# Performance work log

Hardware: AMD Instinct MI355X
Metric: run time of the kernel (lower is better)

Reference implementation:

```python
import jax, jax.numpy as jnp
import numpy as np

HIDDEN = 2560
NUM_HEADS = 32
HEAD = HIDDEN // NUM_HEADS  # 80
ROT = 32                    # partial rotary dim (phi)
THETA = 10000.0
B, S = 2, 2048


def _apply_rope(x, pos):
    """Neox-style rotary embedding on the first ROT dims of the head.
    x: [B, S, H, HEAD], pos: [B, S] int."""
    inv_freq = 1.0 / (THETA ** (jnp.arange(0, ROT, 2, dtype=jnp.float32) / ROT))  # [ROT/2]
    freqs = pos.astype(jnp.float32)[..., None] * inv_freq  # [B, S, ROT/2]
    cos = jnp.cos(freqs)[:, :, None, :].astype(x.dtype)    # [B, S, 1, ROT/2]
    sin = jnp.sin(freqs)[:, :, None, :].astype(x.dtype)
    x_rot, x_pass = x[..., :ROT], x[..., ROT:]
    x1, x2 = x_rot[..., :ROT // 2], x_rot[..., ROT // 2:]
    rotated = jnp.concatenate([x1 * cos - x2 * sin, x2 * cos + x1 * sin], axis=-1)
    return jnp.concatenate([rotated, x_pass], axis=-1)


def setup_inputs() -> dict:
    key = jax.random.key(0)
    k0, k1, k2 = jax.random.split(key, 3)
    hidden_states = jax.random.normal(k0, (B, S, HIDDEN), dtype=jnp.float32)
    position_ids = jnp.broadcast_to(jnp.arange(S, dtype=jnp.int32), (B, S))
    Wqkv_w = jax.random.normal(k1, (3 * HIDDEN, HIDDEN), dtype=jnp.float32) * 0.02
    Wqkv_b = jnp.zeros((3 * HIDDEN,), dtype=jnp.float32)
    out_w = jax.random.normal(k2, (HIDDEN, HIDDEN), dtype=jnp.float32) * 0.02
    out_b = jnp.zeros((HIDDEN,), dtype=jnp.float32)
    return {"position_ids": position_ids, "hidden_states": hidden_states,
            "Wqkv_w": Wqkv_w, "Wqkv_b": Wqkv_b, "out_w": out_w, "out_b": out_b}


def reference(position_ids, hidden_states, Wqkv_w, Wqkv_b, out_w, out_b):
    # Fused QKV projection (torch Linear: y = x @ W^T + b)
    qkv = jnp.einsum('bsh,oh->bso', hidden_states, Wqkv_w) + Wqkv_b  # [B,S,3*HIDDEN]
    q, k, v = jnp.split(qkv, 3, axis=-1)
    q = q.reshape(B, S, NUM_HEADS, HEAD)
    k = k.reshape(B, S, NUM_HEADS, HEAD)
    v = v.reshape(B, S, NUM_HEADS, HEAD)
    # Inline RoPE on q/k (partial, first ROT dims)
    q = _apply_rope(q, position_ids)
    k = _apply_rope(k, position_ids)
    # Causal scaled-dot-product attention (math of the paged prefill kernel)
    scale = HEAD ** -0.5
    scores = jnp.einsum('bqhd,bkhd->bhqk', q, k) * scale  # [B,H,S,S]
    causal = jnp.tril(jnp.ones((S, S), dtype=bool))
    scores = jnp.where(causal, scores, jnp.finfo(scores.dtype).min)
    attn = jax.nn.softmax(scores, axis=-1)
    ctx = jnp.einsum('bhqk,bkhd->bqhd', attn, v).reshape(B, S, HIDDEN)
    return jnp.einsum('bsh,oh->bso', ctx, out_w) + out_b
```

## Files before the change

### kernel.cpp

```cpp
#include <hip/hip_runtime.h>
#include <stdint.h>

#define HIDDEN  2560
#define NHEADS  32
#define HEAD    80
#define QKS     96
#define SEQ     2048
#define BATCH   2
#define M_TOTAL (BATCH*SEQ)
#define QKV_N   (3*HIDDEN)
#define PART_SLOTS 36

typedef __attribute__((ext_vector_type(8))) short  short8;
typedef __attribute__((ext_vector_type(4))) float  floatx4;
typedef __attribute__((ext_vector_type(4))) float  fvec4;
typedef __attribute__((ext_vector_type(4))) unsigned short usvec4;
typedef __attribute__((ext_vector_type(2))) unsigned int uint2v;

#define SBAR() __builtin_amdgcn_sched_barrier(0)

__device__ __forceinline__ unsigned short f2bf(float x){
  union { float f; unsigned u; } v; v.f = x;
  unsigned r = v.u + 0x7fffu + ((v.u >> 16) & 1u);
  return (unsigned short)(r >> 16);
}
__device__ __forceinline__ float bf2f(unsigned short h){
  union { unsigned u; float f; } v; v.u = ((unsigned)h) << 16;
  return v.f;
}
__device__ __forceinline__ unsigned cvt_pk_bf16(float lo, float hi){
  unsigned r;
  asm volatile("v_cvt_pk_bf16_f32 %0, %1, %2" : "=v"(r) : "v"(lo), "v"(hi));
  return r;
}
__device__ __forceinline__ void gload16(const void* g, void* l){
  __builtin_amdgcn_global_load_lds(
    (const __attribute__((address_space(1))) void*)g,
    (__attribute__((address_space(3))) void*)l, 16, 0, 0);
}

__global__ __launch_bounds__(256)
void convert_f32_bf16(const float* __restrict__ src, unsigned short* __restrict__ dst, int n4){
  int idx = blockIdx.x*blockDim.x + threadIdx.x;
  int stride = gridDim.x*blockDim.x;
  for (int i = idx; i < n4; i += stride){
    fvec4 v = *(const fvec4*)(src + (size_t)i*4);
    usvec4 o;
    o[0]=f2bf(v[0]); o[1]=f2bf(v[1]); o[2]=f2bf(v[2]); o[3]=f2bf(v[3]);
    *(usvec4*)(dst + (size_t)i*4) = o;
  }
}

template<bool OUT_BF16>
__global__ __launch_bounds__(512, 2)
void gemm256(const unsigned short* __restrict__ A, const unsigned short* __restrict__ Bm,
             const float* __restrict__ bias, void* __restrict__ Cout,
             int M, int N, int K)
{
  __shared__ __align__(16) unsigned short lds[65536];
  const int tid  = threadIdx.x;
  const int lane = tid & 63;
  const int w    = tid >> 6;
  const int wm   = w >> 2;
  const int wn   = w & 3;
  const int l15  = lane & 15, lg = lane >> 4;

  const int gx  = gridDim.x;
  const int lid = blockIdx.y*gx + blockIdx.x;
  const int nwg = gx*gridDim.y;
  const int qch = nwg >> 3;
  const int sl  = (lid & 7)*qch + (lid >> 3);
  const int bn0 = (sl % gx) * 256;
  const int bm0 = (sl / gx) * 256;

  const int nt = K >> 6;

  int rowq[2], cq[2];
  #pragma unroll
  for (int q=0;q<2;q++){
    int u = (w*2+q)*64 + lane;
    rowq[q] = u >> 2;
    cq[q]   = ((u & 3) - (rowq[q] >> 1)) & 3;
  }
  const int rot = (lg + (l15 >> 1)) & 3;

  floatx4 acc[8][4];
  #pragma unroll
  for (int m=0;m<8;m++)
    #pragma unroll
    for (int n=0;n<4;n++) acc[m][n] = (floatx4)0.0f;

  auto STAGE = [&](int tau, int kkh){
    const int bufb = tau & 1;
    const size_t kofs = (size_t)tau*64 + kkh*32;
    const unsigned sA = (unsigned)(((bufb*2 + 0)*2 + kkh) * 8192);
    const unsigned sB = (unsigned)(((bufb*2 + 1)*2 + kkh) * 8192);
    #pragma unroll
    for (int q=0;q<2;q++){
      gload16(A  + (size_t)(bm0 + rowq[q])*K + kofs + cq[q]*8, &lds[sA + (w*2+q)*512]);
      gload16(Bm + (size_t)(bn0 + rowq[q])*K + kofs + cq[q]*8, &lds[sB + (w*2+q)*512]);
    }
  };
  auto COMPUTE = [&](int bufb, int kkh){
    const unsigned short* As = &lds[((bufb*2+0)*2+kkh)*8192];
    const unsigned short* Bs = &lds[((bufb*2+1)*2+kkh)*8192];
    short8 af[8], bfv[4];
    __builtin_amdgcn_s_setprio(1);
    #pragma unroll
    for (int n=0;n<4;n++)
      bfv[n] = *(const short8*)&Bs[(((wn*64 + n*16 + l15)<<2) + rot)*8];
    #pragma unroll
    for (int m=0;m<8;m++)
      af[m] = *(const short8*)&As[(((wm*128 + m*16 + l15)<<2) + rot)*8];
    #pragma unroll
    for (int m=0;m<8;m++)
      #pragma unroll
      for (int n=0;n<4;n++)
        acc[m][n] = __builtin_amdgcn_mfma_f32_16x16x32_bf16(af[m], bfv[n], acc[m][n], 0, 0, 0);
    __builtin_amdgcn_s_setprio(0);
  };

  STAGE(0,0);
  STAGE(0,1);
  STAGE(1,0);
  asm volatile("s_waitcnt vmcnt(8)" ::: "memory");
  __builtin_amdgcn_s_barrier(); SBAR();

  for (int t=0; t<nt; ++t){
    const int c = t & 1;
    if (t+1 < nt) STAGE(t+1, 1);
    COMPUTE(c, 0);
    if (t+1 < nt) asm volatile("s_waitcnt vmcnt(8)" ::: "memory");
    else          asm volatile("s_waitcnt vmcnt(0)" ::: "memory");
    __builtin_amdgcn_s_barrier(); SBAR();
    if (t+2 < nt) STAGE(t+2, 0);
    COMPUTE(c, 1);
    if (t+1 < nt){
      if (t+2 < nt) asm volatile("s_waitcnt vmcnt(8)" ::: "memory");
      else          asm volatile("s_waitcnt vmcnt(4)" ::: "memory");
      __builtin_amdgcn_s_barrier(); SBAR();
    }
  }

  #pragma unroll
  for (int m=0;m<8;m++){
    #pragma unroll
    for (int n=0;n<4;n++){
      int col = bn0 + wn*64 + n*16 + l15;
      float bs = bias[col];
      #pragma unroll
      for (int r=0;r<4;r++){
        int row = bm0 + wm*128 + m*16 + lg*4 + r;
        float v = acc[m][n][r] + bs;
        if (OUT_BF16) ((unsigned short*)Cout)[(size_t)row*N + col] = f2bf(v);
        else          ((float*)Cout)[(size_t)row*N + col] = v;
      }
    }
  }
}

__global__ __launch_bounds__(256)
void rope_scatter(const unsigned short* __restrict__ qkv,
                  const int* __restrict__ pos_ids,
                  unsigned short* __restrict__ Qp, unsigned short* __restrict__ Kp,
                  unsigned short* __restrict__ Vt)
{
  __shared__ float cosb[128*16];
  __shared__ float sinb[128*16];
  __shared__ __align__(16) unsigned short vtile[128*88];
  const int tid = threadIdx.x;
  const int blk = blockIdx.x;
  const int st = blk & 15, h = (blk >> 4) & 31, b = blk >> 9;
  const int s0 = st*128;

  for (int idx = tid; idx < 128*16; idx += 256){
    int sl = idx >> 4, i = idx & 15;
    float p = (float)pos_ids[b*SEQ + s0 + sl];
    float inv = exp2f(-(float)i * (13.287712379549449f/16.0f));
    float ang = p * inv;
    cosb[idx] = cosf(ang);
    sinb[idx] = sinf(ang);
  }
  __syncthreads();

  const size_t qkrow = (size_t)(b*SEQ + s0)*QKV_N;
  const size_t obase = ((size_t)(b*NHEADS + h)*SEQ + s0)*QKS;
  #pragma unroll
  for (int part = 0; part < 2; part++){
    const int cbase = part*HIDDEN + h*HEAD;
    unsigned short* outp = part ? Kp : Qp;
    for (int idx = tid; idx < 128*QKS; idx += 256){
      int sl = idx / QKS, d = idx - sl*QKS;
      const size_t rb = qkrow + (size_t)sl*QKV_N + cbase;
      float v;
      if (d < 16){
        float x1 = bf2f(qkv[rb + d]);
        float x2 = bf2f(qkv[rb + d + 16]);
        v = x1*cosb[sl*16 + d] - x2*sinb[sl*16 + d];
      } else if (d < 32){
        int i = d - 16;
        float x1 = bf2f(qkv[rb + d - 16]);
        float x2 = bf2f(qkv[rb + d]);
        v = x2*cosb[sl*16 + i] + x1*sinb[sl*16 + i];
      } else if (d < HEAD){
        v = bf2f(qkv[rb + d]);
      } else v = 0.0f;
      outp[obase + (size_t)sl*QKS + d] = f2bf(v);
    }
  }

  for (int idx = tid; idx < 128*HEAD; idx += 256){
    int sl = idx / HEAD, d = idx - sl*HEAD;
    vtile[sl*88 + d] = qkv[qkrow + (size_t)sl*QKV_N + 2*HIDDEN + h*HEAD + d];
  }
  __syncthreads();
  const size_t vtb = ((size_t)(b*NHEADS + h)*HEAD)*SEQ + s0;
  for (int idx = tid; idx < HEAD*128; idx += 256){
    int d = idx >> 7, sl = idx & 127;
    Vt[vtb + (size_t)d*SEQ + sl] = vtile[sl*88 + d];
  }
}

__global__ __launch_bounds__(256, 4)
void attn_fd(const unsigned short* __restrict__ Qp,
             const unsigned short* __restrict__ Kp,
             const unsigned short* __restrict__ Vt,
             unsigned short* __restrict__ ctx,
             unsigned short* __restrict__ pO,
             float* __restrict__ pML)
{
  __shared__ __align__(16) unsigned short Klds[2][64*96];
  __shared__ __align__(16) unsigned short Vlds[2][80*64];
  __shared__ __align__(16) unsigned short p_lds[4][32*36];
  const int tid = threadIdx.x;
  const int lane = tid & 63, w = tid >> 6;
  const int l15 = lane & 15, lg = lane >> 4;

  const int bid = blockIdx.x;
  const int xcd = bid & 7, j = bid >> 3;
  const int bh  = (j/40)*8 + xcd;
  const int tr  = j - (j/40)*40;

  int qt, part, np;
  if (tr < 16)      { qt = 12 + (tr>>2); part = tr & 3; np = 4; }
  else if (tr < 28) { int t = tr-16; int q3 = t/3; qt = 8 + q3; part = t - q3*3; np = 3; }
  else if (tr < 36) { int t = tr-28; qt = 4 + (t>>1); part = t & 1; np = 2; }
  else              { qt = tr - 36; part = 0; np = 1; }
  const int nk  = 2*qt + 2;
  const int kt0 = (part*nk)/np, kt1 = ((part+1)*nk)/np;
  const int q0  = qt*128 + w*32;

  const unsigned short* Qb = Qp + ((size_t)bh*SEQ)*QKS;
  const unsigned short* Kb = Kp + ((size_t)bh*SEQ)*QKS;
  const unsigned short* Vb = Vt + ((size_t)bh*HEAD)*SEQ;

  short8 qf[2][3];
  #pragma unroll
  for (int mi=0; mi<2; mi++)
    #pragma unroll
    for (int kc=0; kc<3; kc++)
      qf[mi][kc] = *(const short8*)&Qb[(size_t)(q0 + mi*16 + l15)*QKS + kc*32 + lg*8];

  int ksrow[3], ksc[3];
  #pragma unroll
  for (int t=0;t<3;t++){
    int ci = (w*3 + t)*64 + lane;
    int row = ci/12, c = ci - row*12;
    ksrow[t] = row;
    ksc[t]   = (c ^ (row & 3))*8;
  }
  int vsrow[3], vsc[3];
  #pragma unroll
  for (int t=0;t<3;t++){
    int i = w + 4*t;
    int row = i*8 + (lane >> 3), c = lane & 7;
    vsrow[t] = row;
    vsc[t]   = (c ^ (row & 7))*8;
  }

  auto STAGE_T = [&](int kt, int bb){
    #pragma unroll
    for (int t=0;t<3;t++)
      gload16(Kb + (size_t)(kt*64 + ksrow[t])*QKS + ksc[t], &Klds[bb][(w*3+t)*512]);
    #pragma unroll
    for (int t=0;t<3;t++){
      int i = w + 4*t;
      if (i < 10)
        gload16(Vb + (size_t)vsrow[t]*SEQ + kt*64 + vsc[t], &Vlds[bb][i*512]);
    }
  };

  float mrun[2] = {-3e38f, -3e38f};
  float lrun[2] = {0.0f, 0.0f};
  floatx4 oacc[2][5];
  #pragma unroll
  for (int mi=0;mi<2;mi++)
    #pragma unroll
    for (int di=0;di<5;di++) oacc[mi][di] = (floatx4)0.0f;

  const float SC = 0.1118033988749895f * 1.4426950408889634f;

  STAGE_T(kt0, 0);
  __syncthreads();

  for (int kt = kt0; kt < kt1; kt++){
    const int cur = (kt - kt0) & 1;
    if (kt+1 < kt1) STAGE_T(kt+1, cur^1);

    if (kt*64 <= q0 + 31){
      floatx4 sacc[2][4];
      #pragma unroll
      for (int mi=0;mi<2;mi++)
        #pragma unroll
        for (int ni=0;ni<4;ni++) sacc[mi][ni] = (floatx4)0.0f;

      __builtin_amdgcn_s_setprio(1);
      #pragma unroll
      for (int kc=0; kc<3; kc++){
        short8 kf[4];
        #pragma unroll
        for (int ni=0; ni<4; ni++){
          int r = ni*16 + l15;
          kf[ni] = *(const short8*)&Klds[cur][r*96 + (((kc*4+lg) ^ (r & 3))<<3)];
        }
        #pragma unroll
        for (int mi=0; mi<2; mi++)
          #pragma unroll
          for (int ni=0; ni<4; ni++)
            sacc[mi][ni] = __builtin_amdgcn_mfma_f32_16x16x32_bf16(kf[ni], qf[mi][kc], sacc[mi][ni], 0, 0, 0);
      }
      __builtin_amdgcn_s_setprio(0);

      if (kt*64 + 63 > q0){
        #pragma unroll
        for (int mi=0; mi<2; mi++){
          int qrow = q0 + mi*16 + l15;
          #pragma unroll
          for (int ni=0; ni<4; ni++){
            int kb = kt*64 + ni*16 + lg*4;
            #pragma unroll
            for (int r=0; r<4; r++)
              if (kb + r > qrow) sacc[mi][ni][r] = -3e38f;
          }
        }
      }

      #pragma unroll
      for (int mi=0; mi<2; mi++){
        float pm = -3e38f;
        #pragma unroll
        for (int ni=0; ni<4; ni++)
          #pragma unroll
          for (int r=0; r<4; r++) pm = fmaxf(pm, sacc[mi][ni][r]);
        pm = fmaxf(pm, __shfl_xor(pm, 16));
        pm = fmaxf(pm, __shfl_xor(pm, 32));
        float mold = mrun[mi];
        float mnew = fmaxf(mold, pm);
        float msc  = mnew*SC;
        float alpha = __builtin_amdgcn_exp2f(mold*SC - msc);
        float rs = 0.0f;
        #pragma unroll
        for (int ni=0; ni<4; ni++)
          #pragma unroll
          for (int r=0; r<4; r++){
            float p = __builtin_amdgcn_exp2f(sacc[mi][ni][r]*SC - msc);
            sacc[mi][ni][r] = p;
            rs += p;
          }
        rs += __shfl_xor(rs, 16);
        rs += __shfl_xor(rs, 32);
        lrun[mi] = lrun[mi]*alpha + rs;
        mrun[mi] = mnew;
        #pragma unroll
        for (int di=0; di<5; di++) oacc[mi][di] *= alpha;
      }

      #pragma unroll
      for (int kk=0; kk<2; kk++){
        #pragma unroll
        for (int mi=0; mi<2; mi++)
          #pragma unroll
          for (int nl=0; nl<2; nl++){
            int ni = kk*2 + nl;
            uint2v pk;
            pk[0] = cvt_pk_bf16(sacc[mi][ni][0], sacc[mi][ni][1]);
            pk[1] = cvt_pk_bf16(sacc[mi][ni][2], sacc[mi][ni][3]);
            *(uint2v*)&p_lds[w][(mi*16 + l15)*36 + nl*16 + lg*4] = pk;
          }
        __builtin_amdgcn_s_setprio(1);
        short8 pa[2];
        #pragma unroll
        for (int mi=0;mi<2;mi++)
          pa[mi] = *(const short8*)&p_lds[w][(mi*16 + l15)*36 + lg*8];
        #pragma unroll
        for (int di=0; di<5; di++){
          int r = di*16 + l15;
          short8 vf = *(const short8*)&Vlds[cur][r*64 + (((kk*4+lg) ^ (r & 7))<<3)];
          #pragma unroll
          for (int mi=0;mi<2;mi++)
            oacc[mi][di] = __builtin_amdgcn_mfma_f32_16x16x32_bf16(vf, pa[mi], oacc[mi][di], 0, 0, 0);
        }
        __builtin_amdgcn_s_setprio(0);
      }
    }
    __syncthreads();
  }

  const int b = bh >> 5, h = bh & 31;
  if (np == 1){
    #pragma unroll
    for (int mi=0;mi<2;mi++){
      float inv = 1.0f/lrun[mi];
      size_t crow = ((size_t)(b*SEQ + q0 + mi*16 + l15))*HIDDEN + h*HEAD;
      #pragma unroll
      for (int di=0;di<5;di++){
        uint2v pk;
        pk[0] = cvt_pk_bf16(oacc[mi][di][0]*inv, oacc[mi][di][1]*inv);
        pk[1] = cvt_pk_bf16(oacc[mi][di][2]*inv, oacc[mi][di][3]*inv);
        *(uint2v*)&ctx[crow + di*16 + lg*4] = pk;
      }
    }
  } else {
    int base;
    if (np == 2)      base = (qt-4)*2;
    else if (np == 3) base = 8 + (qt-8)*3;
    else              base = 20 + (qt-12)*4;
    const int pslot = bh*PART_SLOTS + base + part;
    unsigned short* Ob = pO + (size_t)pslot*128*HEAD;
    #pragma unroll
    for (int mi=0;mi<2;mi++){
      int grow = w*32 + mi*16 + l15;
      #pragma unroll
      for (int di=0;di<5;di++){
        uint2v pk;
        pk[0] = cvt_pk_bf16(oacc[mi][di][0], oacc[mi][di][1]);
        pk[1] = cvt_pk_bf16(oacc[mi][di][2], oacc[mi][di][3]);
        *(uint2v*)&Ob[grow*HEAD + di*16 + lg*4] = pk;
      }
      if (lg == 0){
        float* mlb = pML + ((size_t)pslot*128 + grow)*2;
        mlb[0] = mrun[mi];
        mlb[1] = lrun[mi];
      }
    }
  }
}

__global__ __launch_bounds__(256)
void attn_combine(const unsigned short* __restrict__ pO, const float* __restrict__ pML,
                  unsigned short* __restrict__ ctx)
{
  const int bid = blockIdx.x;
  const int bh = bid / 12, qt = 4 + (bid - (bid/12)*12);
  int base, np;
  if (qt < 8)       { base = (qt-4)*2;       np = 2; }
  else if (qt < 12) { base = 8 + (qt-8)*3;   np = 3; }
  else              { base = 20 + (qt-12)*4; np = 4; }
  const int slot0 = bh*PART_SLOTS + base;
  const float SC = 0.1118033988749895f * 1.4426950408889634f;
  const int b = bh >> 5, h = bh & 31;

  #pragma unroll
  for (int c = 0; c < 5; c++){
    const int e   = c*2048 + threadIdx.x*8;
    const int row = e / 80, d = e - row*80;

    float m[4], l[4], ms = -3e38f;
    for (int p=0;p<np;p++){
      const float* mlb = pML + ((size_t)(slot0+p)*128 + row)*2;
      m[p] = mlb[0]; l[p] = mlb[1];
      ms = fmaxf(ms, m[p]);
    }
    float wgt[4], lsum = 0.0f;
    for (int p=0;p<np;p++){
      wgt[p] = exp2f((m[p]-ms)*SC);
      lsum += wgt[p]*l[p];
    }
    const float inv = 1.0f/lsum;

    float acc[8] = {0,0,0,0,0,0,0,0};
    for (int p=0;p<np;p++){
      short8 v = *(const short8*)&pO[(size_t)(slot0+p)*128*HEAD + e];
      #pragma unroll
      for (int j=0;j<8;j++) acc[j] += wgt[p]*bf2f((unsigned short)v[j]);
    }
    short8 o;
    #pragma unroll
    for (int j=0;j<8;j++) o[j] = (short)f2bf(acc[j]*inv);
    *(short8*)&ctx[((size_t)(b*SEQ + qt*128 + row))*HIDDEN + h*HEAD + d] = o;
  }
}

extern "C" void kernel_launch(void* const* d_in, const int* in_sizes, int n_in,
                              void* d_out, int out_size, void* d_ws, size_t ws_size,
                              hipStream_t stream)
{
  const int*   pos  = (const int*)  d_in[0];
  const float* hid  = (const float*)d_in[1];
  const float* wqkv = (const float*)d_in[2];
  const float* bqkv = (const float*)d_in[3];
  const float* outw = (const float*)d_in[4];
  const float* outb = (const float*)d_in[5];

  char* ws = (char*)d_ws;
  size_t off = 0;
  auto alloc = [&](size_t bytes)->void*{
    void* p = ws + off; off += (bytes + 255) & ~(size_t)255; return p;
  };
  unsigned short* hid_bf  = (unsigned short*)alloc((size_t)M_TOTAL*HIDDEN*2);
  unsigned short* wqkv_bf = (unsigned short*)alloc((size_t)QKV_N*HIDDEN*2);
  unsigned short* outw_bf = (unsigned short*)alloc((size_t)HIDDEN*HIDDEN*2);
  unsigned short* qkv_bf  = (unsigned short*)alloc((size_t)M_TOTAL*QKV_N*2);
  unsigned short* Qp      = (unsigned short*)alloc((size_t)BATCH*NHEADS*SEQ*QKS*2);
  unsigned short* Kp      = (unsigned short*)alloc((size_t)BATCH*NHEADS*SEQ*QKS*2);
  unsigned short* Vt      = (unsigned short*)alloc((size_t)BATCH*NHEADS*HEAD*SEQ*2);
  if (off > ws_size) return;

  unsigned short* pO  = qkv_bf;
  float*          pML = (float*)(qkv_bf + (size_t)64*PART_SLOTS*128*HEAD);

  convert_f32_bf16<<<dim3(1024), dim3(256), 0, stream>>>(hid,  hid_bf,  M_TOTAL*HIDDEN/4);
  convert_f32_bf16<<<dim3(2048), dim3(256), 0, stream>>>(wqkv, wqkv_bf, QKV_N*HIDDEN/4);
  convert_f32_bf16<<<dim3(1024), dim3(256), 0, stream>>>(outw, outw_bf, HIDDEN*HIDDEN/4);

  gemm256<true><<<dim3(QKV_N/256, M_TOTAL/256), dim3(512), 0, stream>>>(
      hid_bf, wqkv_bf, bqkv, (void*)qkv_bf, M_TOTAL, QKV_N, HIDDEN);

  rope_scatter<<<dim3(BATCH*NHEADS*16), dim3(256), 0, stream>>>(qkv_bf, pos, Qp, Kp, Vt);

  unsigned short* ctx = hid_bf;
  attn_fd<<<dim3(2560), dim3(256), 0, stream>>>(Qp, Kp, Vt, ctx, pO, pML);
  attn_combine<<<dim3(64*12), dim3(256), 0, stream>>>(pO, pML, ctx);

  gemm256<false><<<dim3(HIDDEN/256, M_TOTAL/256), dim3(512), 0, stream>>>(
      ctx, outw_bf, outb, d_out, M_TOTAL, HIDDEN, HIDDEN);
}
```

Baseline: 478.2 us.

## Fuse input conversions, remap GEMM tiles per XCD, use 128-tile out-proj GEMM

Merges the three fp32-to-bf16 conversion launches into one kernel to cut launch overhead. Changes the gemm256 workgroup-to-tile mapping so each XCD covers a contiguous 2D block of tiles, aiming for better L2 reuse. Replaces the output-projection GEMM with a new 128x128-tile kernel so more workgroups fill the CUs (the 256-tile version launched only 160 blocks). The new GEMM is simple and unpipelined, with a sync per k-step, which risks lower per-block efficiency. The XCD mapping assumes the grid's x dimension divides by 2 and y by 4.

Result: faster. 462.4 us (median of 2 runs) (-3.3%).

```diff
diff --git a/kernel.cpp b/kernel.cpp
--- a/kernel.cpp
+++ b/kernel.cpp
@@ -40,14 +40,26 @@
 }
 
 __global__ __launch_bounds__(256)
-void convert_f32_bf16(const float* __restrict__ src, unsigned short* __restrict__ dst, int n4){
-  int idx = blockIdx.x*blockDim.x + threadIdx.x;
-  int stride = gridDim.x*blockDim.x;
-  for (int i = idx; i < n4; i += stride){
-    fvec4 v = *(const fvec4*)(src + (size_t)i*4);
-    usvec4 o;
-    o[0]=f2bf(v[0]); o[1]=f2bf(v[1]); o[2]=f2bf(v[2]); o[3]=f2bf(v[3]);
-    *(usvec4*)(dst + (size_t)i*4) = o;
+void convert3(const float* __restrict__ s0, unsigned short* __restrict__ d0, int n0,
+              const float* __restrict__ s1, unsigned short* __restrict__ d1, int n1,
+              const float* __restrict__ s2, unsigned short* __restrict__ d2, int n2)
+{
+  const int idx = blockIdx.x*blockDim.x + threadIdx.x;
+  const int stride = gridDim.x*blockDim.x;
+  for (int i = idx; i < n0; i += stride){
+    fvec4 v = *(const fvec4*)(s0 + (size_t)i*4);
+    usvec4 o; o[0]=f2bf(v[0]); o[1]=f2bf(v[1]); o[2]=f2bf(v[2]); o[3]=f2bf(v[3]);
+    *(usvec4*)(d0 + (size_t)i*4) = o;
+  }
+  for (int i = idx; i < n1; i += stride){
+    fvec4 v = *(const fvec4*)(s1 + (size_t)i*4);
+    usvec4 o; o[0]=f2bf(v[0]); o[1]=f2bf(v[1]); o[2]=f2bf(v[2]); o[3]=f2bf(v[3]);
+    *(usvec4*)(d1 + (size_t)i*4) = o;
+  }
+  for (int i = idx; i < n2; i += stride){
+    fvec4 v = *(const fvec4*)(s2 + (size_t)i*4);
+    usvec4 o; o[0]=f2bf(v[0]); o[1]=f2bf(v[1]); o[2]=f2bf(v[2]); o[3]=f2bf(v[3]);
+    *(usvec4*)(d2 + (size_t)i*4) = o;
   }
 }
 
@@ -67,11 +79,13 @@
 
   const int gx  = gridDim.x;
   const int lid = blockIdx.y*gx + blockIdx.x;
-  const int nwg = gx*gridDim.y;
-  const int qch = nwg >> 3;
-  const int sl  = (lid & 7)*qch + (lid >> 3);
-  const int bn0 = (sl % gx) * 256;
-  const int bm0 = (sl / gx) * 256;
+  const int xcd = lid & 7, jj = lid >> 3;
+  const int bw  = gx >> 1;
+  const int bh2 = gridDim.y >> 2;
+  const int bx  = (xcd & 1)*bw  + jj % bw;
+  const int by  = (xcd >> 1)*bh2 + jj / bw;
+  const int bn0 = bx * 256;
+  const int bm0 = by * 256;
 
   const int nt = K >> 6;
 
@@ -152,6 +166,96 @@
       for (int r=0;r<4;r++){
         int row = bm0 + wm*128 + m*16 + lg*4 + r;
         float v = acc[m][n][r] + bs;
+        if (OUT_BF16) ((unsigned short*)Cout)[(size_t)row*N + col] = f2bf(v);
+        else          ((float*)Cout)[(size_t)row*N + col] = v;
+      }
+    }
+  }
+}
+
+template<bool OUT_BF16>
+__global__ __launch_bounds__(256)
+void gemm_bt(const unsigned short* __restrict__ A, const unsigned short* __restrict__ Bm,
+             const float* __restrict__ bias, void* __restrict__ Cout,
+             int M, int N, int K)
+{
+  __shared__ __align__(16) unsigned short Alds[128*64];
+  __shared__ __align__(16) unsigned short Blds[128*64];
+  const int tid  = threadIdx.x;
+  const int lane = tid & 63;
+  const int wid  = tid >> 6;
+  const int wr   = wid >> 1, wc = wid & 1;
+
+  const int gx  = gridDim.x;
+  const int lid = blockIdx.y*gx + blockIdx.x;
+  const int nwg = gx*gridDim.y;
+  const int qch = nwg >> 3;
+  const int sl  = (lid & 7)*qch + (lid >> 3);
+  const int bx  = sl % gx, by = sl / gx;
+
+  const int rowA0 = by * 128;
+  const int rowB0 = bx * 128;
+  const int l15 = lane & 15, lg = lane >> 4;
+
+  floatx4 acc[4][4];
+  #pragma unroll
+  for (int i=0;i<4;i++)
+    #pragma unroll
+    for (int j=0;j<4;j++) acc[i][j] = (floatx4)0.0f;
+
+  int srow[4], scol[4];
+  #pragma unroll
+  for (int i=0;i<4;i++){
+    int c = wid*4 + i;
+    int e = c*512 + lane*8;
+    int row = e >> 6;
+    int col8 = (e >> 3) & 7;
+    srow[i] = row;
+    scol[i] = ((col8 ^ (row & 7)) << 3);
+  }
+
+  for (int k0 = 0; k0 < K; k0 += 64){
+    #pragma unroll
+    for (int i=0;i<4;i++){
+      int c = wid*4 + i;
+      gload16(A  + (size_t)(rowA0 + srow[i])*K + k0 + scol[i], &Alds[c*512]);
+      gload16(Bm + (size_t)(rowB0 + srow[i])*K + k0 + scol[i], &Blds[c*512]);
+    }
+    __syncthreads();
+    #pragma unroll
+    for (int kk = 0; kk < 64; kk += 32){
+      short8 af[4], bfv[4];
+      #pragma unroll
+      for (int mi=0; mi<4; mi++){
+        int r = wr*64 + mi*16 + l15;
+        int ch = ((kk>>3) + lg) ^ (r & 7);
+        af[mi] = *(const short8*)&Alds[r*64 + ch*8];
+      }
+      #pragma unroll
+      for (int ni=0; ni<4; ni++){
+        int r = wc*64 + ni*16 + l15;
+        int ch = ((kk>>3) + lg) ^ (r & 7);
+        bfv[ni] = *(const short8*)&Blds[r*64 + ch*8];
+      }
+      #pragma unroll
+      for (int mi=0; mi<4; mi++)
+        #pragma unroll
+        for (int ni=0; ni<4; ni++)
+          acc[mi][ni] = __builtin_amdgcn_mfma_f32_16x16x32_bf16(af[mi], bfv[ni], acc[mi][ni], 0, 0, 0);
+    }
+    __syncthreads();
+  }
+
+  #pragma unroll
+  for (int mi=0; mi<4; mi++){
+    #pragma unroll
+    for (int ni=0; ni<4; ni++){
+      int col = rowB0 + wc*64 + ni*16 + l15;
+      float bs = bias[col];
+      #pragma unroll
+      for (int r=0;r<4;r++){
+        int row = rowA0 + wr*64 + mi*16 + lg*4 + r;
+        float v = acc[mi][ni][r] + bs;
         if (OUT_BF16) ((unsigned short*)Cout)[(size_t)row*N + col] = f2bf(v);
         else          ((float*)Cout)[(size_t)row*N + col] = v;
       }
@@ -519,9 +623,10 @@
   unsigned short* pO  = qkv_bf;
   float*          pML = (float*)(qkv_bf + (size_t)64*PART_SLOTS*128*HEAD);
 
-  convert_f32_bf16<<<dim3(1024), dim3(256), 0, stream>>>(hid,  hid_bf,  M_TOTAL*HIDDEN/4);
-  convert_f32_bf16<<<dim3(2048), dim3(256), 0, stream>>>(wqkv, wqkv_bf, QKV_N*HIDDEN/4);
-  convert_f32_bf16<<<dim3(1024), dim3(256), 0, stream>>>(outw, outw_bf, HIDDEN*HIDDEN/4);
+  convert3<<<dim3(2048), dim3(256), 0, stream>>>(
+      hid,  hid_bf,  M_TOTAL*HIDDEN/4,
+      wqkv, wqkv_bf, QKV_N*HIDDEN/4,
+      outw, outw_bf, HIDDEN*HIDDEN/4);
 
   gemm256<true><<<dim3(QKV_N/256, M_TOTAL/256), dim3(512), 0, stream>>>(
       hid_bf, wqkv_bf, bqkv, (void*)qkv_bf, M_TOTAL, QKV_N, HIDDEN);
@@ -532,6 +637,6 @@
   attn_fd<<<dim3(2560), dim3(256), 0, stream>>>(Qp, Kp, Vt, ctx, pO, pML);
   attn_combine<<<dim3(64*12), dim3(256), 0, stream>>>(pO, pML, ctx);
 
-  gemm256<false><<<dim3(HIDDEN/256, M_TOTAL/256), dim3(512), 0, stream>>>(
+  gemm_bt<false><<<dim3(HIDDEN/128, M_TOTAL/128), dim3(256), 0, stream>>>(
       ctx, outw_bf, outb, d_out, M_TOTAL, HIDDEN, HIDDEN);
 }
```
